# Performance work log

Hardware: AMD Instinct MI355X
Metric: run time of the kernel (lower is better)

The kernel has to match this reference:

```python
import jax, jax.numpy as jnp
import numpy as np
from jax import lax

N, M, K = 192, 192, 3
B, H, W = 16, 16, 16
MK = M * K


def _deconv(x, w, b):
    # PyTorch ConvTranspose2d(k=5, stride=2, padding=2, output_padding=1)
    # == dilated conv with flipped kernel, pads (k-1-p, k-1-p+op) = (2, 3)
    wt = jnp.flip(w, (2, 3)).transpose(1, 0, 2, 3)  # (in,out,kh,kw) -> (out,in,kh,kw)
    y = lax.conv_general_dilated(x, wt, (1, 1), [(2, 3), (2, 3)],
                                 lhs_dilation=(2, 2),
                                 dimension_numbers=('NCHW', 'OIHW', 'NCHW'))
    return y + b[None, :, None, None]


def _conv(x, w, b, pad):
    y = lax.conv_general_dilated(x, w, (1, 1), [(pad, pad), (pad, pad)],
                                 dimension_numbers=('NCHW', 'OIHW', 'NCHW'))
    return y + b[None, :, None, None]


def _leaky(x):
    return jnp.where(x >= 0, x, 0.01 * x)


def setup_inputs() -> dict:
    key = jax.random.key(0)
    ks = jax.random.split(key, 19)
    s = 0.02
    d = {
        'z1': jax.random.normal(ks[0], (B, N, H, W), jnp.float32),
        # gmm_sigma branch
        'gs_w1': jax.random.normal(ks[1], (N, N, 5, 5), jnp.float32) * s,
        'gs_b1': jnp.zeros((N,), jnp.float32),
        'gs_w2': jax.random.normal(ks[2], (N, N, 5, 5), jnp.float32) * s,
        'gs_b2': jnp.zeros((N,), jnp.float32),
        'gs_w3': jax.random.normal(ks[3], (MK, N, 5, 5), jnp.float32) * s,
        'gs_b3': jnp.zeros((MK,), jnp.float32),
        # gmm_means branch
        'gm_w1': jax.random.normal(ks[4], (N, N, 5, 5), jnp.float32) * s,
        'gm_b1': jnp.zeros((N,), jnp.float32),
        'gm_w2': jax.random.normal(ks[5], (N, N, 5, 5), jnp.float32) * s,
        'gm_b2': jnp.zeros((N,), jnp.float32),
        'gm_w3': jax.random.normal(ks[6], (MK, N, 5, 5), jnp.float32) * s,
        'gm_b3': jnp.zeros((MK,), jnp.float32),
        # gmm_weights branch
        'gw_w1': jax.random.normal(ks[7], (N, N, 5, 5), jnp.float32) * s,
        'gw_b1': jnp.zeros((N,), jnp.float32),
        'gw_w2': jax.random.normal(ks[8], (N, MK, 5, 5), jnp.float32) * s,
        'gw_b2': jnp.zeros((MK,), jnp.float32),
        'gw_w3': jax.random.normal(ks[9], (MK, MK, 1, 1), jnp.float32) * s,
        'gw_b3': jnp.zeros((MK,), jnp.float32),
    }
    return d


def reference(z1, gs_w1, gs_b1, gs_w2, gs_b2, gs_w3, gs_b3,
              gm_w1, gm_b1, gm_w2, gm_b2, gm_w3, gm_b3,
              gw_w1, gw_b1, gw_w2, gw_b2, gw_w3, gw_b3):
    # sigma: deconv, ReLU, deconv, ReLU, conv(k5,s1), ReLU
    s = jax.nn.relu(_deconv(z1, gs_w1, gs_b1))
    s = jax.nn.relu(_deconv(s, gs_w2, gs_b2))
    sigma = jax.nn.relu(_conv(s, gs_w3, gs_b3, 2))
    # means: deconv, LeakyReLU, deconv, LeakyReLU, conv(k5,s1)
    m = _leaky(_deconv(z1, gm_w1, gm_b1))
    m = _leaky(_deconv(m, gm_w2, gm_b2))
    means = _conv(m, gm_w3, gm_b3, 2)
    # weights: deconv, LeakyReLU, deconv, global-max-pool, LeakyReLU, conv1x1
    w = _leaky(_deconv(z1, gw_w1, gw_b1))
    w = _deconv(w, gw_w2, gw_b2)
    w = jnp.max(w, axis=(2, 3), keepdims=True)  # fused replacement of the B*C python loop
    w = _leaky(w)
    w = _conv(w, gw_w3, gw_b3, 0)  # (B, M*K, 1, 1)
    temp = w.reshape(-1, K, M, 1, 1)
    temp = jax.nn.softmax(temp, axis=1)  # softmax over the K mixture components
    weights = temp.reshape(-1, MK, 1, 1)
    return (sigma, means, weights)
```

## Files before the change

kernel.cpp:

```cpp
#include <hip/hip_runtime.h>
#include <hip/hip_bf16.h>
#include <math.h>

typedef __attribute__((ext_vector_type(8))) short bf16x8;
typedef __attribute__((ext_vector_type(4))) float f32x4;
typedef __attribute__((ext_vector_type(16))) float f32x16;
typedef __attribute__((ext_vector_type(4))) unsigned short ushort4v;

constexpr int Bsz = 16;

__device__ __forceinline__ float act_r(float v, int a) {
  if (a == 1) return v > 0.f ? v : 0.f;
  if (a == 2) return v >= 0.f ? v : 0.01f * v;
  return v;
}

__device__ __forceinline__ unsigned short f2bf(float x) {
  __hip_bfloat16 h = __float2bfloat16(x);
  return __builtin_bit_cast(unsigned short, h);
}

__device__ __forceinline__ void gll16(const unsigned short* g, unsigned short* l) {
  __builtin_amdgcn_global_load_lds(
      (const __attribute__((address_space(1))) unsigned int*)g,
      (__attribute__((address_space(3))) unsigned int*)l, 16, 0, 0);
}

__global__ __launch_bounds__(256) void zprep_k(
    const float* __restrict__ z, unsigned short* __restrict__ zh)
{
  const int g = blockIdx.x * 256 + threadIdx.x;
  if (g >= 16 * 192 * 256) return;
  const int b  = g / 49152;
  const int rr = g - b * 49152;
  const int px = rr / 192;
  const int ic = rr - px * 192;
  const int o = ((b * 6 + (ic >> 5)) * 256 + px) * 32 + (ic & 31);
  zh[o] = f2bf(z[(b * 192 + ic) * 256 + px]);
}

__device__ __forceinline__ void dprep_one(
    const float* __restrict__ w, unsigned short* __restrict__ wh, int OC, int g)
{
  const int oc  = g % OC;
  const int rem = g / OC;
  const int icb = rem % 24;
  const int j   = rem / 24;
  bf16x8 hv;
  #pragma unroll
  for (int e = 0; e < 8; ++e)
    hv[e] = (short)f2bf(w[((icb * 8 + e) * OC + oc) * 25 + j]);
  *(bf16x8*)&wh[((j * 24 + icb) * OC + oc) * 8] = hv;
}

__global__ __launch_bounds__(256) void wprep1_k(
    const float* __restrict__ s0, const float* __restrict__ s1,
    const float* __restrict__ s2, unsigned short* __restrict__ wh)
{
  const int bid = blockIdx.x;
  const int seg = bid / 450;
  const int g   = (bid - seg * 450) * 256 + threadIdx.x;
  if (g >= 192 * 24 * 25) return;
  const float* src = seg == 0 ? s0 : (seg == 1 ? s1 : s2);
  dprep_one(src, wh + (size_t)seg * 921600, 192, g);
}

__global__ __launch_bounds__(256) void wprep_d_k(
    const float* __restrict__ w, unsigned short* __restrict__ wh, int OC)
{
  const int g = blockIdx.x * 256 + threadIdx.x;
  if (g >= OC * 24 * 25) return;
  dprep_one(w, wh, OC, g);
}

__global__ __launch_bounds__(256) void wprep_t_k(
    const float* __restrict__ w, unsigned short* __restrict__ wh)
{
  const int g = blockIdx.x * 256 + threadIdx.x;
  if (g >= 576 * 24 * 25) return;
  const int oc  = g % 576;
  const int rem = g / 576;
  const int icb = rem % 24;
  const int j   = rem / 24;
  bf16x8 hv;
  #pragma unroll
  for (int e = 0; e < 8; ++e)
    hv[e] = (short)f2bf(w[oc * 4800 + (icb * 8 + e) * 25 + j]);
  *(bf16x8*)&wh[((j * 24 + icb) * 576 + oc) * 8] = hv;
}

template<int H, int OMODE, int OL, int RPW>
__global__ __launch_bounds__(256, 2) void deconv2_k(
    const unsigned short* __restrict__ xh, long x_brs,
    const unsigned short* __restrict__ wh, long w_brs,
    const float* __restrict__ b0, const float* __restrict__ b1,
    const float* __restrict__ b2,
    unsigned short* __restrict__ yh, long y_brs,
    float* __restrict__ mvp, int OC, int a0, int a1, int a2)
{
  constexpr int NF = H / 16;
  constexpr int R  = 4 * RPW;
  __shared__ __align__(16) unsigned short xs[R + 2][H + 2][32];
  __shared__ float red[4][32];

  const int zz = blockIdx.z;
  const int br = zz >> 4;
  const int b  = zz & 15;
  const int by = blockIdx.y;
  const int r0 = by * R;
  const int oc0 = blockIdx.x * 32;
  const int t  = threadIdx.x;
  const int wv = t >> 6;
  const int l  = t & 63;
  const int lg = l >> 4;
  const int ln = l & 15;

  const unsigned short* xhp = xh + (long)br * x_brs;
  const unsigned short* whp = wh + (long)br * w_brs;
  const float* bias = br == 0 ? b0 : (br == 1 ? b1 : b2);
  const int act = br == 0 ? a0 : (br == 1 ? a1 : a2);

  f32x4 acc[RPW][4][2][NF];
  #pragma unroll
  for (int rr = 0; rr < RPW; ++rr)
    #pragma unroll
    for (int p = 0; p < 4; ++p)
      #pragma unroll
      for (int of = 0; of < 2; ++of)
        #pragma unroll
        for (int nf = 0; nf < NF; ++nf)
          acc[rr][p][of][nf] = (f32x4){0.f, 0.f, 0.f, 0.f};

  const bf16x8 zero8 = {0,0,0,0,0,0,0,0};

  for (int c = 0; c < 6; ++c) {
    __syncthreads();
    constexpr int DC = (R + 2) * H * 4;
    #pragma unroll
    for (int k = 0; k < (DC + 255) / 256; ++k) {
      const int li = t + k * 256;
      if (li < DC) {
        const int part = li & 3;
        const int col  = (li >> 2) & (H - 1);
        const int row  = li / (4 * H);
        const int y    = r0 - 1 + row;
        bf16x8 v = zero8;
        if ((unsigned)y < (unsigned)H)
          v = *(const bf16x8*)&xhp[(((size_t)(b * 6 + c) * H + y) * H + col) * 32 + part * 8];
        *(bf16x8*)&xs[row][col + 1][part * 8] = v;
      }
    }
    if (t < 8 * (R + 2)) {
      const int row = t >> 3;
      const int cc  = t & 7;
      const int col = (cc >> 2) ? (H + 1) : 0;
      *(bf16x8*)&xs[row][col][(cc & 3) * 8] = zero8;
    }
    __syncthreads();

    #pragma unroll
    for (int j = 0; j < 25; ++j) {
      const int ky = j / 5, kx = j % 5;
      const int sy = ky & 1, sx = kx & 1;
      const int dy = (2 + sy - ky) / 2;
      const int dx = (2 + sx - kx) / 2;
      const int p  = sy * 2 + sx;

      bf16x8 ah[2];
      const int wbase = ((j * 24 + c * 4 + lg) * OC + oc0 + ln) * 8;
      #pragma unroll
      for (int of = 0; of < 2; ++of)
        ah[of] = *(const bf16x8*)&whp[wbase + of * 128];
      #pragma unroll
      for (int rr = 0; rr < RPW; ++rr) {
        const int rl = RPW * wv + rr + 1 + dy;
        bf16x8 bh[NF];
        #pragma unroll
        for (int nf = 0; nf < NF; ++nf) {
          const int cl = 1 + nf * 16 + ln + dx;
          bh[nf] = *(const bf16x8*)&xs[rl][cl][lg * 8];
        }
        #pragma unroll
        for (int of = 0; of < 2; ++of)
          #pragma unroll
          for (int nf = 0; nf < NF; ++nf)
            acc[rr][p][of][nf] = __builtin_amdgcn_mfma_f32_16x16x32_bf16(
                ah[of], bh[nf], acc[rr][p][of][nf], 0, 0, 0);
      }
    }
  }

  if (OMODE == 1) {
    const int OCG = OC >> 5;
    float bv[2][4];
    #pragma unroll
    for (int of = 0; of < 2; ++of)
      #pragma unroll
      for (int r = 0; r < 4; ++r)
        bv[of][r] = bias[oc0 + of * 16 + lg * 4 + r];
    unsigned short* yhp = yh + (long)br * y_brs;
    #pragma unroll
    for (int rr = 0; rr < RPW; ++rr) {
      const int iy = r0 + RPW * wv + rr;
      #pragma unroll
      for (int sy = 0; sy < 2; ++sy)
        #pragma unroll
        for (int sx = 0; sx < 2; ++sx) {
          const int p  = sy * 2 + sx;
          const int oy = 2 * iy + sy;
          #pragma unroll
          for (int of = 0; of < 2; ++of) {
            const int ocb = oc0 + of * 16 + lg * 4;
            const int cg  = ocb >> 5;
            const int co  = ocb & 31;
            #pragma unroll
            for (int nf = 0; nf < NF; ++nf) {
              const int ox = 2 * (nf * 16 + ln) + sx;
              ushort4v hv;
              #pragma unroll
              for (int r = 0; r < 4; ++r)
                hv[r] = f2bf(act_r(acc[rr][p][of][nf][r] + bv[of][r], act));
              size_t idx;
              if (OL) {
                const int qg = cg * 4 + (co >> 3);
                idx = (((size_t)(b * (OC >> 3) + qg) * (4 * H * H)) +
                       (size_t)oy * (2 * H) + ox) * 8 + (co & 7);
              } else {
                idx = (((size_t)(b * OCG + cg) * (4 * H * H)) +
                       (size_t)oy * (2 * H) + ox) * 32 + co;
              }
              *(ushort4v*)&yhp[idx] = hv;
            }
          }
        }
    }
  } else {
    #pragma unroll
    for (int of = 0; of < 2; ++of)
      #pragma unroll
      for (int r = 0; r < 4; ++r) {
        float m = -3.402823466e38f;
        #pragma unroll
        for (int rr = 0; rr < RPW; ++rr)
          #pragma unroll
          for (int p = 0; p < 4; ++p)
            #pragma unroll
            for (int nf = 0; nf < NF; ++nf)
              m = fmaxf(m, acc[rr][p][of][nf][r]);
        #pragma unroll
        for (int off = 1; off < 16; off <<= 1)
          m = fmaxf(m, __shfl_xor(m, off));
        if (ln == 0)
          red[wv][of * 16 + lg * 4 + r] = m + bias[oc0 + of * 16 + lg * 4 + r];
      }
    __syncthreads();
    if (t < 32) {
      const float v = fmaxf(fmaxf(red[0][t], red[1][t]), fmaxf(red[2][t], red[3][t]));
      mvp[((b * 4) + by) * OC + oc0 + t] = v;
    }
  }
}

__global__ __launch_bounds__(256, 3) void conv3_k(
    const unsigned short* __restrict__ gxh,
    const unsigned short* __restrict__ gwh,
    const float* __restrict__ bias, float* __restrict__ out, int act)
{
  __shared__ __align__(16) unsigned short xs[8][4][80][8];

  const int bid  = blockIdx.x;
  const int orig = (bid & 7) * 288 + (bid >> 3);
  const int ocg  = orig >> 8;
  const int rem  = orig & 255;
  const int b    = rem >> 4;
  const int band = rem & 15;
  const int y0   = band * 4;
  const int oc0  = ocg * 64;
  const int t    = threadIdx.x;
  const int wv   = t >> 6;
  const int l    = t & 63;
  const int lg   = l >> 4;
  const int ln   = l & 15;

  f32x4 acc[4][4];
  #pragma unroll
  for (int of = 0; of < 4; ++of)
    #pragma unroll
    for (int pf = 0; pf < 4; ++pf)
      acc[of][pf] = (f32x4){0.f, 0.f, 0.f, 0.f};

  int ky2v[5], rlv[5];
  #pragma unroll
  for (int ky = 0; ky < 5; ++ky) {
    int k2 = ky + wv; if (k2 >= 5) k2 -= 5;
    ky2v[ky] = k2; rlv[ky] = wv + k2;
  }

  {
    unsigned short* fx = (unsigned short*)xs;
    const bf16x8 z8 = {0,0,0,0,0,0,0,0};
    #pragma unroll
    for (int k = 0; k < 10; ++k) {
      const int li = t + k * 256;
      if (li < 2560) *(bf16x8*)&fx[li * 8] = z8;
    }
  }

  for (int c = 0; c < 6; ++c) {
    __syncthreads();
    #pragma unroll
    for (int k = 0; k < 8; ++k) {
      const int idx = k * 4 + wv;
      const int row = idx >> 2, q = idx & 3;
      const int y = y0 - 2 + row;
      if ((unsigned)y < 64u) {
        const unsigned short* g = &gxh[
            ((((size_t)b * 24 + c * 4 + q) << 12) + ((size_t)y << 6) + l) * 8];
        gll16(g, &xs[row][q][2][0]);
      }
    }
    __syncthreads();

    const unsigned short* wrow = gwh + ((size_t)((c * 4 + lg) * 576) + oc0 + ln) * 8;
    const unsigned short* xrow[5];
    #pragma unroll
    for (int ky = 0; ky < 5; ++ky)
      xrow[ky] = &xs[rlv[ky]][lg][ln][0];

    bf16x8 ah[2][4], bx[2][4];

    #define LDW(KY, KX, S)                                                  \
      {                                                                     \
        const unsigned short* wj = wrow + (size_t)(ky2v[KY] * 5 + (KX)) * 110592; \
        _Pragma("unroll")                                                   \
        for (int of = 0; of < 4; ++of)                                      \
          ah[S][of] = *(const bf16x8*)&wj[of * 128];                        \
        const unsigned short* xr = xrow[KY];                                \
        _Pragma("unroll")                                                   \
        for (int pf = 0; pf < 4; ++pf)                                      \
          bx[S][pf] = *(const bf16x8*)&xr[(pf * 16 + (KX)) * 8];            \
      }

    LDW(0, 0, 0)
    #pragma unroll
    for (int j = 0; j < 25; ++j) {
      const int s = j & 1;
      if (j < 24) {
        const int jn = j + 1;
        const int kyn = jn / 5, kxn = jn % 5;
        const int ns = jn & 1;
        LDW(kyn, kxn, ns)
      }
      __builtin_amdgcn_s_setprio(1);
      #pragma unroll
      for (int of = 0; of < 4; ++of)
        #pragma unroll
        for (int pf = 0; pf < 4; ++pf)
          acc[of][pf] = __builtin_amdgcn_mfma_f32_16x16x32_bf16(
              ah[s][of], bx[s][pf], acc[of][pf], 0, 0, 0);
      __builtin_amdgcn_s_setprio(0);
    }
    #undef LDW
  }

  const int y = y0 + wv;
  #pragma unroll
  for (int of = 0; of < 4; ++of)
    #pragma unroll
    for (int r = 0; r < 4; ++r) {
      const int oc = oc0 + of * 16 + lg * 4 + r;
      const float bv = bias[oc];
      float* po = &out[(((size_t)(b * 576 + oc) * 64) + y) * 64 + ln];
      #pragma unroll
      for (int pf = 0; pf < 4; ++pf)
        po[16 * pf] = act_r(acc[of][pf][r] + bv, act);
    }
}

__global__ __launch_bounds__(256) void head_k(
    const float* __restrict__ mvp, const float* __restrict__ w3,
    const float* __restrict__ b3, float* __restrict__ outw)
{
  __shared__ float lv[576];
  __shared__ float yv[576];
  const int b = blockIdx.x;
  const int t = threadIdx.x;
  for (int i = t; i < 576; i += 256) {
    float m = mvp[(b * 4 + 0) * 576 + i];
    #pragma unroll
    for (int ti = 1; ti < 4; ++ti)
      m = fmaxf(m, mvp[(b * 4 + ti) * 576 + i]);
    lv[i] = m >= 0.f ? m : 0.01f * m;
  }
  __syncthreads();
  for (int oc = t; oc < 576; oc += 256) {
    float s = b3[oc];
    for (int c = 0; c < 576; ++c) s += w3[oc * 576 + c] * lv[c];
    yv[oc] = s;
  }
  __syncthreads();
  if (t < 192) {
    const float v0 = yv[t], v1 = yv[192 + t], v2 = yv[384 + t];
    const float mx = fmaxf(v0, fmaxf(v1, v2));
    const float e0 = expf(v0 - mx), e1 = expf(v1 - mx), e2 = expf(v2 - mx);
    const float inv = 1.f / (e0 + e1 + e2);
    outw[b * 576 + t]       = e0 * inv;
    outw[b * 576 + 192 + t] = e1 * inv;
    outw[b * 576 + 384 + t] = e2 * inv;
  }
}

extern "C" void kernel_launch(void* const* d_in, const int* in_sizes, int n_in,
                              void* d_out, int out_size, void* d_ws, size_t ws_size,
                              hipStream_t stream)
{
  (void)in_sizes; (void)n_in; (void)out_size; (void)ws_size;

  const float* z1    = (const float*)d_in[0];
  const float* gs_w1 = (const float*)d_in[1];
  const float* gs_b1 = (const float*)d_in[2];
  const float* gs_w2 = (const float*)d_in[3];
  const float* gs_b2 = (const float*)d_in[4];
  const float* gs_w3 = (const float*)d_in[5];
  const float* gs_b3 = (const float*)d_in[6];
  const float* gm_w1 = (const float*)d_in[7];
  const float* gm_b1 = (const float*)d_in[8];
  const float* gm_w2 = (const float*)d_in[9];
  const float* gm_b2 = (const float*)d_in[10];
  const float* gm_w3 = (const float*)d_in[11];
  const float* gm_b3 = (const float*)d_in[12];
  const float* gw_w1 = (const float*)d_in[13];
  const float* gw_b1 = (const float*)d_in[14];
  const float* gw_w2 = (const float*)d_in[15];
  const float* gw_b2 = (const float*)d_in[16];
  const float* gw_w3 = (const float*)d_in[17];
  const float* gw_b3 = (const float*)d_in[18];

  unsigned short* p = (unsigned short*)d_ws;
  unsigned short* Z   = p; p += 786432;
  unsigned short* A1  = p; p += (size_t)3 * 3145728;
  unsigned short* A2  = p; p += 12582912;
  unsigned short* W1  = p; p += (size_t)3 * 921600;
  unsigned short* Wb  = p; p += 2764800;
  float* MVp = (float*)p;

  float* o_sigma = (float*)d_out;
  float* o_means = o_sigma + (size_t)Bsz * 576 * 64 * 64;
  float* o_w     = o_means + (size_t)Bsz * 576 * 64 * 64;

  dim3 blk(256);

  zprep_k<<<dim3(3072), blk, 0, stream>>>(z1, Z);
  wprep1_k<<<dim3(1350), blk, 0, stream>>>(gs_w1, gm_w1, gw_w1, W1);

  deconv2_k<16,1,0,2><<<dim3(6,2,48), blk, 0, stream>>>(
      Z, 0, W1, 921600, gs_b1, gm_b1, gw_b1,
      A1, 3145728, nullptr, 192, 1, 2, 2);

  wprep_d_k<<<dim3(450), blk, 0, stream>>>(gs_w2, Wb, 192);
  deconv2_k<32,1,1,1><<<dim3(6,8,16), blk, 0, stream>>>(
      A1, 0, Wb, 0, gs_b2, gs_b2, gs_b2,
      A2, 0, nullptr, 192, 1, 1, 1);
  wprep_t_k<<<dim3(1350), blk, 0, stream>>>(gs_w3, Wb);
  conv3_k<<<dim3(2304), blk, 0, stream>>>(A2, Wb, gs_b3, o_sigma, 1);

  wprep_d_k<<<dim3(450), blk, 0, stream>>>(gm_w2, Wb, 192);
  deconv2_k<32,1,1,1><<<dim3(6,8,16), blk, 0, stream>>>(
      A1 + (size_t)3145728, 0, Wb, 0, gm_b2, gm_b2, gm_b2,
      A2, 0, nullptr, 192, 2, 2, 2);
  wprep_t_k<<<dim3(1350), blk, 0, stream>>>(gm_w3, Wb);
  conv3_k<<<dim3(2304), blk, 0, stream>>>(A2, Wb, gm_b3, o_means, 0);

  wprep_d_k<<<dim3(1350), blk, 0, stream>>>(gw_w2, Wb, 576);
  deconv2_k<32,2,0,2><<<dim3(18,4,16), blk, 0, stream>>>(
      A1 + (size_t)2 * 3145728, 0, Wb, 0,
      gw_b2, gw_b2, gw_b2, nullptr, 0, MVp, 576, 0, 0, 0);
  head_k<<<dim3(16), blk, 0, stream>>>(MVp, gw_w3, gw_b3, o_w);
}
```

Measured before the change: 1.044 ms.

## Switch conv3 to 32x32x16 MFMA and restructure deconv LDS layout and tap order

The final 5x5 conv now uses 32x32x16 bf16 MFMA with two K sub-steps per tap instead of 16x16x32 tiles. Its LDS tile is padded (84 columns) to cut bank conflicts. The deconv kernel stores its input tile channel-group-major with padding, zero-fills once instead of per chunk, and visits taps grouped by parity with a per-wave rotated row order so waves stagger their LDS reads. The stride-2 deconvs now use two rows per wave with half the blocks, trading occupancy and register pressure for more weight reuse.

```diff
diff --git a/kernel.cpp b/kernel.cpp
--- a/kernel.cpp
+++ b/kernel.cpp
@@ -100,7 +100,8 @@
 {
   constexpr int NF = H / 16;
   constexpr int R  = 4 * RPW;
-  __shared__ __align__(16) unsigned short xs[R + 2][H + 2][32];
+  constexpr int PC = (H == 16) ? 20 : 36;
+  __shared__ __align__(16) unsigned short xs[R + 2][4][PC][8];
   __shared__ float red[4][32];
 
   const int zz = blockIdx.z;
@@ -131,7 +132,30 @@
         for (int nf = 0; nf < NF; ++nf)
           acc[rr][p][of][nf] = (f32x4){0.f, 0.f, 0.f, 0.f};
 
+  int evv[3], odv[2];
+  {
+    const int ev0[3] = {0, 2, 4};
+    const int od0[2] = {1, 3};
+    const int er = wv % 3, orr = wv & 1;
+    #pragma unroll
+    for (int i = 0; i < 3; ++i) { int ii = i + er; if (ii >= 3) ii -= 3; evv[i] = ev0[ii]; }
+    #pragma unroll
+    for (int i = 0; i < 2; ++i) { int ii = i + orr; if (ii >= 2) ii -= 2; odv[i] = od0[ii]; }
+  }
+
+  {
+    unsigned short* fx = (unsigned short*)xs;
+    constexpr int ZL = (R + 2) * 4 * PC;
+    const bf16x8 z8 = {0,0,0,0,0,0,0,0};
+    #pragma unroll
+    for (int k = 0; k < (ZL + 255) / 256; ++k) {
+      const int li = t + k * 256;
+      if (li < ZL) *(bf16x8*)&fx[li * 8] = z8;
+    }
+  }
+
   const bf16x8 zero8 = {0,0,0,0,0,0,0,0};
+  (void)zero8;
 
   for (int c = 0; c < 6; ++c) {
     __syncthreads();
@@ -144,50 +168,59 @@
         const int col  = (li >> 2) & (H - 1);
         const int row  = li / (4 * H);
         const int y    = r0 - 1 + row;
-        bf16x8 v = zero8;
-        if ((unsigned)y < (unsigned)H)
-          v = *(const bf16x8*)&xhp[(((size_t)(b * 6 + c) * H + y) * H + col) * 32 + part * 8];
-        *(bf16x8*)&xs[row][col + 1][part * 8] = v;
+        if ((unsigned)y < (unsigned)H) {
+          const bf16x8 v = *(const bf16x8*)&xhp[
+              (((size_t)(b * 6 + c) * H + y) * H + col) * 32 + part * 8];
+          *(bf16x8*)&xs[row][part][col + 1][0] = v;
+        }
       }
     }
-    if (t < 8 * (R + 2)) {
-      const int row = t >> 3;
-      const int cc  = t & 7;
-      const int col = (cc >> 2) ? (H + 1) : 0;
-      *(bf16x8*)&xs[row][col][(cc & 3) * 8] = zero8;
-    }
     __syncthreads();
 
-    #pragma unroll
-    for (int j = 0; j < 25; ++j) {
-      const int ky = j / 5, kx = j % 5;
-      const int sy = ky & 1, sx = kx & 1;
-      const int dy = (2 + sy - ky) / 2;
-      const int dx = (2 + sx - kx) / 2;
-      const int p  = sy * 2 + sx;
-
-      bf16x8 ah[2];
-      const int wbase = ((j * 24 + c * 4 + lg) * OC + oc0 + ln) * 8;
-      #pragma unroll
-      for (int of = 0; of < 2; ++of)
-        ah[of] = *(const bf16x8*)&whp[wbase + of * 128];
-      #pragma unroll
-      for (int rr = 0; rr < RPW; ++rr) {
-        const int rl = RPW * wv + rr + 1 + dy;
-        bf16x8 bh[NF];
-        #pragma unroll
-        for (int nf = 0; nf < NF; ++nf) {
-          const int cl = 1 + nf * 16 + ln + dx;
-          bh[nf] = *(const bf16x8*)&xs[rl][cl][lg * 8];
-        }
-        #pragma unroll
-        for (int of = 0; of < 2; ++of)
-          #pragma unroll
-          for (int nf = 0; nf < NF; ++nf)
-            acc[rr][p][of][nf] = __builtin_amdgcn_mfma_f32_16x16x32_bf16(
-                ah[of], bh[nf], acc[rr][p][of][nf], 0, 0, 0);
+    #define TAP_BODY(KY2, DY, P, KX)                                        \
+      {                                                                     \
+        const int jT = (KY2) * 5 + (KX);                                    \
+        const int dxT = 1 - ((KX) >> 1);                                    \
+        bf16x8 ahT[2];                                                      \
+        const int wbaseT = ((jT * 24 + c * 4 + lg) * OC + oc0 + ln) * 8;    \
+        _Pragma("unroll")                                                   \
+        for (int of = 0; of < 2; ++of)                                      \
+          ahT[of] = *(const bf16x8*)&whp[wbaseT + of * 128];                \
+        _Pragma("unroll")                                                   \
+        for (int rr = 0; rr < RPW; ++rr) {                                  \
+          const int rlT = RPW * wv + rr + 1 + (DY);                         \
+          bf16x8 bhT[NF];                                                   \
+          _Pragma("unroll")                                                 \
+          for (int nf = 0; nf < NF; ++nf)                                   \
+            bhT[nf] = *(const bf16x8*)&xs[rlT][lg][1 + nf * 16 + ln + dxT][0]; \
+          __builtin_amdgcn_s_setprio(1);                                    \
+          _Pragma("unroll")                                                 \
+          for (int of = 0; of < 2; ++of)                                    \
+            _Pragma("unroll")                                               \
+            for (int nf = 0; nf < NF; ++nf)                                 \
+              acc[rr][P][of][nf] = __builtin_amdgcn_mfma_f32_16x16x32_bf16( \
+                  ahT[of], bhT[nf], acc[rr][P][of][nf], 0, 0, 0);           \
+          __builtin_amdgcn_s_setprio(0);                                    \
+        }                                                                   \
       }
-    }
+
+    #pragma unroll
+    for (int ki = 0; ki < 3; ++ki) {
+      const int ky2 = evv[ki];
+      const int dy  = 1 - (ky2 >> 1);
+      #pragma unroll
+      for (int kx = 0; kx < 5; ++kx)
+        TAP_BODY(ky2, dy, (kx & 1), kx)
+    }
+    #pragma unroll
+    for (int ki = 0; ki < 2; ++ki) {
+      const int ky2 = odv[ki];
+      const int dy  = 1 - (ky2 >> 1);
+      #pragma unroll
+      for (int kx = 0; kx < 5; ++kx)
+        TAP_BODY(ky2, dy, (2 + (kx & 1)), kx)
+    }
+    #undef TAP_BODY
   }
 
   if (OMODE == 1) {
@@ -266,7 +299,7 @@
     const unsigned short* __restrict__ gwh,
     const float* __restrict__ bias, float* __restrict__ out, int act)
 {
-  __shared__ __align__(16) unsigned short xs[8][4][80][8];
+  __shared__ __align__(16) unsigned short xs[8][4][84][8];
 
   const int bid  = blockIdx.x;
   const int orig = (bid & 7) * 288 + (bid >> 3);
@@ -279,15 +312,17 @@
   const int t    = threadIdx.x;
   const int wv   = t >> 6;
   const int l    = t & 63;
-  const int lg   = l >> 4;
-  const int ln   = l & 15;
-
-  f32x4 acc[4][4];
+  const int lh   = l >> 5;
+  const int ln5  = l & 31;
+
+  f32x16 acc[2][2];
   #pragma unroll
-  for (int of = 0; of < 4; ++of)
-    #pragma unroll
-    for (int pf = 0; pf < 4; ++pf)
-      acc[of][pf] = (f32x4){0.f, 0.f, 0.f, 0.f};
+  for (int of = 0; of < 2; ++of)
+    #pragma unroll
+    for (int pf = 0; pf < 2; ++pf)
+      #pragma unroll
+      for (int r = 0; r < 16; ++r)
+        acc[of][pf][r] = 0.f;
 
   int ky2v[5], rlv[5];
   #pragma unroll
@@ -300,9 +335,9 @@
     unsigned short* fx = (unsigned short*)xs;
     const bf16x8 z8 = {0,0,0,0,0,0,0,0};
     #pragma unroll
-    for (int k = 0; k < 10; ++k) {
+    for (int k = 0; k < 11; ++k) {
       const int li = t + k * 256;
-      if (li < 2560) *(bf16x8*)&fx[li * 8] = z8;
+      if (li < 2688) *(bf16x8*)&fx[li * 8] = z8;
     }
   }
 
@@ -321,24 +356,28 @@
     }
     __syncthreads();
 
-    const unsigned short* wrow = gwh + ((size_t)((c * 4 + lg) * 576) + oc0 + ln) * 8;
-    const unsigned short* xrow[5];
+    const unsigned short* wrow = gwh + ((size_t)((c * 4 + lh) * 576) + oc0 + ln5) * 8;
+    const unsigned short* xb[5];
     #pragma unroll
     for (int ky = 0; ky < 5; ++ky)
-      xrow[ky] = &xs[rlv[ky]][lg][ln][0];
-
-    bf16x8 ah[2][4], bx[2][4];
+      xb[ky] = &xs[rlv[ky]][lh][ln5][0];
+
+    bf16x8 ah[2][2][2], bx[2][2][2];
 
     #define LDW(KY, KX, S)                                                  \
       {                                                                     \
-        const unsigned short* wj = wrow + (size_t)(ky2v[KY] * 5 + (KX)) * 110592; \
+        const size_t jo = (size_t)(ky2v[KY] * 5 + (KX)) * 110592;           \
         _Pragma("unroll")                                                   \
-        for (int of = 0; of < 4; ++of)                                      \
-          ah[S][of] = *(const bf16x8*)&wj[of * 128];                        \
-        const unsigned short* xr = xrow[KY];                                \
+        for (int kk = 0; kk < 2; ++kk)                                      \
+          _Pragma("unroll")                                                 \
+          for (int of = 0; of < 2; ++of)                                    \
+            ah[S][kk][of] = *(const bf16x8*)&wrow[jo + kk * 9216 + of * 256]; \
+        const unsigned short* xr = xb[KY];                                  \
         _Pragma("unroll")                                                   \
-        for (int pf = 0; pf < 4; ++pf)                                      \
-          bx[S][pf] = *(const bf16x8*)&xr[(pf * 16 + (KX)) * 8];            \
+        for (int kk = 0; kk < 2; ++kk)                                      \
+          _Pragma("unroll")                                                 \
+          for (int pf = 0; pf < 2; ++pf)                                    \
+            bx[S][kk][pf] = *(const bf16x8*)&xr[kk * 1344 + (pf * 32 + (KX)) * 8]; \
       }
 
     LDW(0, 0, 0)
@@ -347,17 +386,17 @@
       const int s = j & 1;
       if (j < 24) {
         const int jn = j + 1;
-        const int kyn = jn / 5, kxn = jn % 5;
-        const int ns = jn & 1;
-        LDW(kyn, kxn, ns)
+        LDW(jn / 5, jn % 5, jn & 1)
       }
       __builtin_amdgcn_s_setprio(1);
       #pragma unroll
-      for (int of = 0; of < 4; ++of)
+      for (int kk = 0; kk < 2; ++kk)
         #pragma unroll
-        for (int pf = 0; pf < 4; ++pf)
-          acc[of][pf] = __builtin_amdgcn_mfma_f32_16x16x32_bf16(
-              ah[s][of], bx[s][pf], acc[of][pf], 0, 0, 0);
+        for (int of = 0; of < 2; ++of)
+          #pragma unroll
+          for (int pf = 0; pf < 2; ++pf)
+            acc[of][pf] = __builtin_amdgcn_mfma_f32_32x32x16_bf16(
+                ah[s][kk][of], bx[s][kk][pf], acc[of][pf], 0, 0, 0);
       __builtin_amdgcn_s_setprio(0);
     }
     #undef LDW
@@ -365,15 +404,15 @@
 
   const int y = y0 + wv;
   #pragma unroll
-  for (int of = 0; of < 4; ++of)
-    #pragma unroll
-    for (int r = 0; r < 4; ++r) {
-      const int oc = oc0 + of * 16 + lg * 4 + r;
+  for (int of = 0; of < 2; ++of)
+    #pragma unroll
+    for (int r = 0; r < 16; ++r) {
+      const int oc = oc0 + of * 32 + (r & 3) + 8 * (r >> 2) + 4 * lh;
       const float bv = bias[oc];
-      float* po = &out[(((size_t)(b * 576 + oc) * 64) + y) * 64 + ln];
-      #pragma unroll
-      for (int pf = 0; pf < 4; ++pf)
-        po[16 * pf] = act_r(acc[of][pf][r] + bv, act);
+      float* po = &out[(((size_t)(b * 576 + oc) * 64) + y) * 64 + ln5];
+      #pragma unroll
+      for (int pf = 0; pf < 2; ++pf)
+        po[32 * pf] = act_r(acc[of][pf][r] + bv, act);
     }
 }
 
@@ -458,14 +497,14 @@
       A1, 3145728, nullptr, 192, 1, 2, 2);
 
   wprep_d_k<<<dim3(450), blk, 0, stream>>>(gs_w2, Wb, 192);
-  deconv2_k<32,1,1,1><<<dim3(6,8,16), blk, 0, stream>>>(
+  deconv2_k<32,1,1,2><<<dim3(6,4,16), blk, 0, stream>>>(
       A1, 0, Wb, 0, gs_b2, gs_b2, gs_b2,
       A2, 0, nullptr, 192, 1, 1, 1);
   wprep_t_k<<<dim3(1350), blk, 0, stream>>>(gs_w3, Wb);
   conv3_k<<<dim3(2304), blk, 0, stream>>>(A2, Wb, gs_b3, o_sigma, 1);
 
   wprep_d_k<<<dim3(450), blk, 0, stream>>>(gm_w2, Wb, 192);
-  deconv2_k<32,1,1,1><<<dim3(6,8,16), blk, 0, stream>>>(
+  deconv2_k<32,1,1,2><<<dim3(6,4,16), blk, 0, stream>>>(
       A1 + (size_t)3145728, 0, Wb, 0, gm_b2, gm_b2, gm_b2,
       A2, 0, nullptr, 192, 2, 2, 2);
   wprep_t_k<<<dim3(1350), blk, 0, stream>>>(gm_w3, Wb);
```

After: 1.129 ms. 1.08x slower.
